# Performance work log

Measured on AMD Instinct MI355X. Metric: run time of the kernel, lower is better.

Reference implementation:

```python
import jax, jax.numpy as jnp
import numpy as np

G = 128          # number of point-cloud groups
DOWNSAMPLE = 256 # points per group
D = 256          # feature dim


def _pairwise_dist(x, y):
    # x: [G, n, d], y: [G, m, d] -> Euclidean distances [G, n, m]
    x2 = jnp.sum(x * x, axis=-1)[:, :, None]
    y2 = jnp.sum(y * y, axis=-1)[:, None, :]
    d2 = jnp.maximum(x2 + y2 - 2.0 * jnp.einsum('gnd,gmd->gnm', x, y), 0.0)
    # safe sqrt (zero diagonal has zero distance, avoid NaN grads)
    return jnp.where(d2 > 0, jnp.sqrt(jnp.where(d2 > 0, d2, 1.0)), 0.0)


def setup_inputs() -> dict:
    key = jax.random.key(0)
    k1, k2 = jax.random.split(key)
    inp = jax.random.normal(k1, (G * DOWNSAMPLE, D), dtype=jnp.float32)
    tgt = jax.random.normal(k2, (G * DOWNSAMPLE, D), dtype=jnp.float32)
    return {"input": inp, "target": tgt, "downsample": DOWNSAMPLE}


def reference(input, target, downsample):
    # MMDLoss.forward: reshape to (-1, downsample, D), batched energy distance, mean
    x = input.reshape(-1, downsample, input.shape[-1])   # [G, n, D]
    y = target.reshape(-1, downsample, target.shape[-1]) # [G, m, D]
    # Energy distance (geomloss 'energy' kernel k(x,y) = -||x-y||, uniform weights):
    # L = mean_ij ||x_i - y_j|| - 0.5 mean_ij ||x_i - x_j|| - 0.5 mean_ij ||y_i - y_j||
    d_xy = jnp.mean(_pairwise_dist(x, y), axis=(1, 2))  # [G]
    d_xx = jnp.mean(_pairwise_dist(x, x), axis=(1, 2))  # [G]
    d_yy = jnp.mean(_pairwise_dist(y, y), axis=(1, 2))  # [G]
    loss_per_group = d_xy - 0.5 * d_xx - 0.5 * d_yy
    return jnp.mean(loss_per_group)
```

## Files before the change

kernel.cpp:

```cpp
#include <hip/hip_runtime.h>
#include <hip/hip_bf16.h>
#include <stdint.h>
#include <string.h>

typedef __attribute__((ext_vector_type(8))) short short8;
typedef __attribute__((ext_vector_type(4))) float floatx4;

#define NPTS 256
#define DIM  256
#define TILE 128
#define BK   32
#define NIT  (DIM / BK)

static __device__ __forceinline__ uint32_t cvtsq2(float a, float b, float& s) {
    __hip_bfloat162 h = __float22bfloat162_rn(float2{a, b});
    uint32_t d;
    memcpy(&d, &h, 4);
    const float lo = __builtin_bit_cast(float, d << 16);
    const float hi = __builtin_bit_cast(float, d & 0xFFFF0000u);
    s += lo * lo + hi * hi;
    return d;
}

__global__ __launch_bounds__(512, 4)
void mmd_pipe(const float* __restrict__ X, const float* __restrict__ Y,
              float* __restrict__ out, float scale, int G) {
    int g, t;
    const int f = blockIdx.x;
    if ((G & 7) == 0) { const int xcd = f & 7, j = f >> 3; g = (j / 10) * 8 + xcd; t = j % 10; }
    else              { g = f / 10; t = f % 10; }

    int ptype, ti, tj; float w;
    if (t < 4)      { ptype = 0; ti = t >> 1; tj = t & 1; w = 1.0f; }
    else if (t < 7) { int u = t - 4; ptype = 1; ti = (u == 2); tj = (u >= 1); w = (u == 1) ? -1.0f : -0.5f; }
    else            { int u = t - 7; ptype = 2; ti = (u == 2); tj = (u >= 1); w = (u == 1) ? -1.0f : -0.5f; }

    const float *Pf, *Qf;
    if (ptype == 0)      { Pf = X; Qf = Y; }
    else if (ptype == 1) { Pf = X; Qf = X; }
    else                 { Pf = Y; Qf = Y; }
    const bool symdiag = (ptype != 0) && (ti == tj);

    const size_t prow0 = (size_t)g * NPTS + (size_t)ti * TILE;
    const size_t qrow0 = (size_t)g * NPTS + (size_t)tj * TILE;

    __shared__ __align__(16) uint16_t As[2][TILE * BK];
    __shared__ __align__(16) uint16_t Bs[2][TILE * BK];
    __shared__ float rnorm[TILE];
    __shared__ float cnorm[TILE];
    __shared__ float wpart[8];

    const int tid  = threadIdx.x;
    const int lane = tid & 63;
    const int wv   = tid >> 6;
    const int quad = lane >> 4;
    const int l15  = lane & 15;
    const int rowbase = (wv & 3) * 32;
    const int colbase = (wv >> 2) * 64;
    const int rsw = (quad ^ ((l15 >> 1) & 3)) * 8;

    const int prow = tid >> 2;
    const int pchk = tid & 3;
    const float* gA = Pf + (prow0 + prow) * DIM + pchk * 8;
    const float* gB = Qf + (qrow0 + prow) * DIM + pchk * 8;
    const int woff = prow * BK + ((pchk ^ ((prow >> 1) & 3)) * 8);

    floatx4 acc[2][4];
    #pragma unroll
    for (int i = 0; i < 2; ++i)
        #pragma unroll
        for (int j = 0; j < 4; ++j) acc[i][j] = (floatx4)0.0f;

    float sqp = 0.0f, sqq = 0.0f;

    float4 ra0 = *(const float4*)(gA);
    float4 ra1 = *(const float4*)(gA + 4);
    float4 rb0 = *(const float4*)(gB);
    float4 rb1 = *(const float4*)(gB + 4);
    {
        uint4 pa, pb;
        pa.x = cvtsq2(ra0.x, ra0.y, sqp); pa.y = cvtsq2(ra0.z, ra0.w, sqp);
        pa.z = cvtsq2(ra1.x, ra1.y, sqp); pa.w = cvtsq2(ra1.z, ra1.w, sqp);
        pb.x = cvtsq2(rb0.x, rb0.y, sqq); pb.y = cvtsq2(rb0.z, rb0.w, sqq);
        pb.z = cvtsq2(rb1.x, rb1.y, sqq); pb.w = cvtsq2(rb1.z, rb1.w, sqq);
        *(uint4*)&As[0][woff] = pa;
        *(uint4*)&Bs[0][woff] = pb;
    }
    ra0 = *(const float4*)(gA + BK);
    ra1 = *(const float4*)(gA + BK + 4);
    rb0 = *(const float4*)(gB + BK);
    rb1 = *(const float4*)(gB + BK + 4);

    #pragma unroll
    for (int it = 0; it < NIT; ++it) {
        const int b = it & 1;
        __syncthreads();

        if (it < NIT - 1) {
            uint4 pa, pb;
            pa.x = cvtsq2(ra0.x, ra0.y, sqp); pa.y = cvtsq2(ra0.z, ra0.w, sqp);
            pa.z = cvtsq2(ra1.x, ra1.y, sqp); pa.w = cvtsq2(ra1.z, ra1.w, sqp);
            pb.x = cvtsq2(rb0.x, rb0.y, sqq); pb.y = cvtsq2(rb0.z, rb0.w, sqq);
            pb.z = cvtsq2(rb1.x, rb1.y, sqq); pb.w = cvtsq2(rb1.z, rb1.w, sqq);
            *(uint4*)&As[b ^ 1][woff] = pa;
            *(uint4*)&Bs[b ^ 1][woff] = pb;
        }
        if (it < NIT - 2) {
            const int k0 = (it + 2) * BK;
            ra0 = *(const float4*)(gA + k0);
            ra1 = *(const float4*)(gA + k0 + 4);
            rb0 = *(const float4*)(gB + k0);
            rb1 = *(const float4*)(gB + k0 + 4);
        }

        short8 af[2], bfr[4];
        #pragma unroll
        for (int mi = 0; mi < 2; ++mi)
            af[mi] = *(const short8*)&As[b][(rowbase + mi * 16 + l15) * BK + rsw];
        #pragma unroll
        for (int ni = 0; ni < 4; ++ni)
            bfr[ni] = *(const short8*)&Bs[b][(colbase + ni * 16 + l15) * BK + rsw];
        #pragma unroll
        for (int mi = 0; mi < 2; ++mi)
            #pragma unroll
            for (int ni = 0; ni < 4; ++ni)
                acc[mi][ni] = __builtin_amdgcn_mfma_f32_16x16x32_bf16(
                    af[mi], bfr[ni], acc[mi][ni], 0, 0, 0);
    }

    sqp += __shfl_xor(sqp, 1); sqp += __shfl_xor(sqp, 2);
    sqq += __shfl_xor(sqq, 1); sqq += __shfl_xor(sqq, 2);
    if ((tid & 3) == 0) { rnorm[prow] = sqp; cnorm[prow] = sqq; }
    __syncthreads();

    float lsum = 0.0f;
    #pragma unroll
    for (int mi = 0; mi < 2; ++mi) {
        #pragma unroll
        for (int i = 0; i < 4; ++i) {
            const int r = rowbase + mi * 16 + quad * 4 + i;
            const float rv = rnorm[r];
            #pragma unroll
            for (int ni = 0; ni < 4; ++ni) {
                const int c = colbase + ni * 16 + l15;
                float d2 = rv + cnorm[c] - 2.0f * acc[mi][ni][i];
                float s = sqrtf(fmaxf(d2, 0.0f));
                if (symdiag && (r == c)) s = 0.0f;
                lsum += s;
            }
        }
    }
    #pragma unroll
    for (int off = 32; off; off >>= 1) lsum += __shfl_down(lsum, off);
    if (lane == 0) wpart[wv] = lsum;
    __syncthreads();
    if (tid == 0) {
        float bs = 0.0f;
        #pragma unroll
        for (int i = 0; i < 8; ++i) bs += wpart[i];
        atomicAdd(out, bs * (w * scale));
    }
}

extern "C" void kernel_launch(void* const* d_in, const int* in_sizes, int n_in,
                              void* d_out, int out_size, void* d_ws, size_t ws_size,
                              hipStream_t stream) {
    const float* X = (const float*)d_in[0];
    const float* Y = (const float*)d_in[1];
    const int total_elems = in_sizes[0];
    const int G = total_elems / (NPTS * DIM);

    float* out = (float*)d_out;
    hipMemsetAsync(out, 0, sizeof(float) * out_size, stream);

    const float scale = 1.0f / ((float)NPTS * (float)NPTS * (float)G);
    mmd_pipe<<<10 * G, 512, 0, stream>>>(X, Y, out, scale, G);
}
```

Before: 124.6 us.

## Stage full K panel in LDS once, then run MFMA loop without barriers

The kernel now loads and converts the entire 256-wide K dimension of both tiles into LDS up front (128 KB total) and then runs all MFMA steps without per-iteration barriers, in place of the double-buffered pipelined loop. Symmetric diagonal tiles load only the P tile and reuse it as B. Norms are now computed from the fp32 values rather than the bf16-rounded ones, and LDS is reused for the norms and partial sums. In exchange, the much larger LDS footprint lowers occupancy (launch bounds drop to 2) and load latency no longer overlaps with MFMA work.

```diff
diff --git a/kernel.cpp b/kernel.cpp
--- a/kernel.cpp
+++ b/kernel.cpp
@@ -11,19 +11,21 @@
 #define TILE 128
 #define BK   32
 #define NIT  (DIM / BK)
+#define SLICE (TILE * BK)
 
-static __device__ __forceinline__ uint32_t cvtsq2(float a, float b, float& s) {
+static __device__ __forceinline__ uint32_t cvt2(float a, float b) {
     __hip_bfloat162 h = __float22bfloat162_rn(float2{a, b});
     uint32_t d;
     memcpy(&d, &h, 4);
-    const float lo = __builtin_bit_cast(float, d << 16);
-    const float hi = __builtin_bit_cast(float, d & 0xFFFF0000u);
-    s += lo * lo + hi * hi;
     return d;
 }
+static __device__ __forceinline__ float sq8(const float4 u, const float4 v) {
+    return u.x * u.x + u.y * u.y + u.z * u.z + u.w * u.w +
+           v.x * v.x + v.y * v.y + v.z * v.z + v.w * v.w;
+}
 
-__global__ __launch_bounds__(512, 4)
-void mmd_pipe(const float* __restrict__ X, const float* __restrict__ Y,
+__global__ __launch_bounds__(512, 2)
+void mmd_mono(const float* __restrict__ X, const float* __restrict__ Y,
               float* __restrict__ out, float scale, int G) {
     int g, t;
     const int f = blockIdx.x;
@@ -44,11 +46,9 @@
     const size_t prow0 = (size_t)g * NPTS + (size_t)ti * TILE;
     const size_t qrow0 = (size_t)g * NPTS + (size_t)tj * TILE;
 
-    __shared__ __align__(16) uint16_t As[2][TILE * BK];
-    __shared__ __align__(16) uint16_t Bs[2][TILE * BK];
-    __shared__ float rnorm[TILE];
-    __shared__ float cnorm[TILE];
-    __shared__ float wpart[8];
+    __shared__ __align__(16) uint16_t As[NIT][SLICE];
+    __shared__ __align__(16) uint16_t Bs[NIT][SLICE];
+    float* nsh = (float*)&As[0][0];
 
     const int tid  = threadIdx.x;
     const int lane = tid & 63;
@@ -62,8 +62,58 @@
     const int prow = tid >> 2;
     const int pchk = tid & 3;
     const float* gA = Pf + (prow0 + prow) * DIM + pchk * 8;
-    const float* gB = Qf + (qrow0 + prow) * DIM + pchk * 8;
     const int woff = prow * BK + ((pchk ^ ((prow >> 1) & 3)) * 8);
+
+    float sqp = 0.0f, sqq = 0.0f;
+
+    if (symdiag) {
+        float4 a0 = *(const float4*)(gA);
+        float4 a1 = *(const float4*)(gA + 4);
+        #pragma unroll
+        for (int s = 0; s < NIT; ++s) {
+            float4 na0, na1;
+            if (s < NIT - 1) {
+                na0 = *(const float4*)(gA + (s + 1) * BK);
+                na1 = *(const float4*)(gA + (s + 1) * BK + 4);
+            }
+            sqp += sq8(a0, a1);
+            uint4 pa;
+            pa.x = cvt2(a0.x, a0.y); pa.y = cvt2(a0.z, a0.w);
+            pa.z = cvt2(a1.x, a1.y); pa.w = cvt2(a1.z, a1.w);
+            *(uint4*)&As[s][woff] = pa;
+            if (s < NIT - 1) { a0 = na0; a1 = na1; }
+        }
+    } else {
+        const float* gB = Qf + (qrow0 + prow) * DIM + pchk * 8;
+        float4 a0 = *(const float4*)(gA);
+        float4 a1 = *(const float4*)(gA + 4);
+        float4 b0 = *(const float4*)(gB);
+        float4 b1 = *(const float4*)(gB + 4);
+        #pragma unroll
+        for (int s = 0; s < NIT; ++s) {
+            float4 na0, na1, nb0, nb1;
+            if (s < NIT - 1) {
+                na0 = *(const float4*)(gA + (s + 1) * BK);
+                na1 = *(const float4*)(gA + (s + 1) * BK + 4);
+                nb0 = *(const float4*)(gB + (s + 1) * BK);
+                nb1 = *(const float4*)(gB + (s + 1) * BK + 4);
+            }
+            sqp += sq8(a0, a1);
+            sqq += sq8(b0, b1);
+            uint4 pa, pb;
+            pa.x = cvt2(a0.x, a0.y); pa.y = cvt2(a0.z, a0.w);
+            pa.z = cvt2(a1.x, a1.y); pa.w = cvt2(a1.z, a1.w);
+            pb.x = cvt2(b0.x, b0.y); pb.y = cvt2(b0.z, b0.w);
+            pb.z = cvt2(b1.x, b1.y); pb.w = cvt2(b1.z, b1.w);
+            *(uint4*)&As[s][woff] = pa;
+            *(uint4*)&Bs[s][woff] = pb;
+            if (s < NIT - 1) { a0 = na0; a1 = na1; b0 = nb0; b1 = nb1; }
+        }
+    }
+    sqp += __shfl_xor(sqp, 1); sqp += __shfl_xor(sqp, 2);
+    sqq += __shfl_xor(sqq, 1); sqq += __shfl_xor(sqq, 2);
+
+    __syncthreads();
 
     floatx4 acc[2][4];
     #pragma unroll
@@ -71,55 +121,18 @@
         #pragma unroll
         for (int j = 0; j < 4; ++j) acc[i][j] = (floatx4)0.0f;
 
-    float sqp = 0.0f, sqq = 0.0f;
-
-    float4 ra0 = *(const float4*)(gA);
-    float4 ra1 = *(const float4*)(gA + 4);
-    float4 rb0 = *(const float4*)(gB);
-    float4 rb1 = *(const float4*)(gB + 4);
-    {
-        uint4 pa, pb;
-        pa.x = cvtsq2(ra0.x, ra0.y, sqp); pa.y = cvtsq2(ra0.z, ra0.w, sqp);
-        pa.z = cvtsq2(ra1.x, ra1.y, sqp); pa.w = cvtsq2(ra1.z, ra1.w, sqp);
-        pb.x = cvtsq2(rb0.x, rb0.y, sqq); pb.y = cvtsq2(rb0.z, rb0.w, sqq);
-        pb.z = cvtsq2(rb1.x, rb1.y, sqq); pb.w = cvtsq2(rb1.z, rb1.w, sqq);
-        *(uint4*)&As[0][woff] = pa;
-        *(uint4*)&Bs[0][woff] = pb;
-    }
-    ra0 = *(const float4*)(gA + BK);
-    ra1 = *(const float4*)(gA + BK + 4);
-    rb0 = *(const float4*)(gB + BK);
-    rb1 = *(const float4*)(gB + BK + 4);
-
+    const uint16_t* bbase = symdiag ? &As[0][0] : &Bs[0][0];
     #pragma unroll
     for (int it = 0; it < NIT; ++it) {
-        const int b = it & 1;
-        __syncthreads();
-
-        if (it < NIT - 1) {
-            uint4 pa, pb;
-            pa.x = cvtsq2(ra0.x, ra0.y, sqp); pa.y = cvtsq2(ra0.z, ra0.w, sqp);
-            pa.z = cvtsq2(ra1.x, ra1.y, sqp); pa.w = cvtsq2(ra1.z, ra1.w, sqp);
-            pb.x = cvtsq2(rb0.x, rb0.y, sqq); pb.y = cvtsq2(rb0.z, rb0.w, sqq);
-            pb.z = cvtsq2(rb1.x, rb1.y, sqq); pb.w = cvtsq2(rb1.z, rb1.w, sqq);
-            *(uint4*)&As[b ^ 1][woff] = pa;
-            *(uint4*)&Bs[b ^ 1][woff] = pb;
-        }
-        if (it < NIT - 2) {
-            const int k0 = (it + 2) * BK;
-            ra0 = *(const float4*)(gA + k0);
-            ra1 = *(const float4*)(gA + k0 + 4);
-            rb0 = *(const float4*)(gB + k0);
-            rb1 = *(const float4*)(gB + k0 + 4);
-        }
-
+        const uint16_t* ab = &As[it][0];
+        const uint16_t* bb = bbase + it * SLICE;
         short8 af[2], bfr[4];
         #pragma unroll
         for (int mi = 0; mi < 2; ++mi)
-            af[mi] = *(const short8*)&As[b][(rowbase + mi * 16 + l15) * BK + rsw];
+            af[mi] = *(const short8*)&ab[(rowbase + mi * 16 + l15) * BK + rsw];
         #pragma unroll
         for (int ni = 0; ni < 4; ++ni)
-            bfr[ni] = *(const short8*)&Bs[b][(colbase + ni * 16 + l15) * BK + rsw];
+            bfr[ni] = *(const short8*)&bb[(colbase + ni * 16 + l15) * BK + rsw];
         #pragma unroll
         for (int mi = 0; mi < 2; ++mi)
             #pragma unroll
@@ -128,9 +141,11 @@
                     af[mi], bfr[ni], acc[mi][ni], 0, 0, 0);
     }
 
-    sqp += __shfl_xor(sqp, 1); sqp += __shfl_xor(sqp, 2);
-    sqq += __shfl_xor(sqq, 1); sqq += __shfl_xor(sqq, 2);
-    if ((tid & 3) == 0) { rnorm[prow] = sqp; cnorm[prow] = sqq; }
+    __syncthreads();
+    if ((tid & 3) == 0) {
+        nsh[prow] = sqp;
+        nsh[TILE + prow] = symdiag ? sqp : sqq;
+    }
     __syncthreads();
 
     float lsum = 0.0f;
@@ -139,11 +154,11 @@
         #pragma unroll
         for (int i = 0; i < 4; ++i) {
             const int r = rowbase + mi * 16 + quad * 4 + i;
-            const float rv = rnorm[r];
+            const float rv = nsh[r];
             #pragma unroll
             for (int ni = 0; ni < 4; ++ni) {
                 const int c = colbase + ni * 16 + l15;
-                float d2 = rv + cnorm[c] - 2.0f * acc[mi][ni][i];
+                float d2 = rv + nsh[TILE + c] - 2.0f * acc[mi][ni][i];
                 float s = sqrtf(fmaxf(d2, 0.0f));
                 if (symdiag && (r == c)) s = 0.0f;
                 lsum += s;
@@ -152,12 +167,12 @@
     }
     #pragma unroll
     for (int off = 32; off; off >>= 1) lsum += __shfl_down(lsum, off);
-    if (lane == 0) wpart[wv] = lsum;
+    if (lane == 0) nsh[2 * TILE + wv] = lsum;
     __syncthreads();
     if (tid == 0) {
         float bs = 0.0f;
         #pragma unroll
-        for (int i = 0; i < 8; ++i) bs += wpart[i];
+        for (int i = 0; i < 8; ++i) bs += nsh[2 * TILE + i];
         atomicAdd(out, bs * (w * scale));
     }
 }
@@ -174,5 +189,5 @@
     hipMemsetAsync(out, 0, sizeof(float) * out_size, stream);
 
     const float scale = 1.0f / ((float)NPTS * (float)NPTS * (float)G);
-    mmd_pipe<<<10 * G, 512, 0, stream>>>(X, Y, out, scale, G);
+    mmd_mono<<<10 * G, 512, 0, stream>>>(X, Y, out, scale, G);
 }
```

After: 121.7 us. 2.3% less time.
